# Performance work log

Hardware: AMD Instinct MI355X
Metric: run time of the kernel (lower is better)

## Reference

```python
import jax, jax.numpy as jnp
import numpy as np

N, M, E = 100000, 20000, 500000
D = 128
NNZ_E, NNZ_V = 200000, 500000


def _seg_mean(x, idx, num):
    s = jax.ops.segment_sum(x, idx, num_segments=num)
    cnt = jax.ops.segment_sum(jnp.ones((x.shape[0], 1), x.dtype), idx, num_segments=num)
    return s / jnp.maximum(cnt, 1.0)


def _spmm(row, col, val, x, num_rows):
    # COO sparse-dense matmul: out[r] = sum_nnz val * x[c]
    return jax.ops.segment_sum(val[:, None] * x[col], row, num_segments=num_rows)


def setup_inputs() -> dict:
    key = jax.random.key(0)
    ks = jax.random.split(key, 18)
    s = 0.05
    return {
        "vfeat": jax.random.normal(ks[0], (N, D), jnp.float32),
        "efeat": jax.random.normal(ks[1], (M, D), jnp.float32),
        "invDV": jax.random.uniform(ks[2], (N,), jnp.float32, 0.01, 1.0),
        "invDE": jax.random.uniform(ks[3], (M,), jnp.float32, 0.01, 1.0),
        "inc_v": jax.random.randint(ks[4], (E,), 0, N, jnp.int32),
        "inc_e": jax.random.randint(ks[5], (E,), 0, M, jnp.int32),
        "eMat_row": jax.random.randint(ks[6], (NNZ_E,), 0, M, jnp.int32),
        "eMat_col": jax.random.randint(ks[7], (NNZ_E,), 0, M, jnp.int32),
        "eMat_val": jax.random.normal(ks[8], (NNZ_E,), jnp.float32) * s,
        "vMat_row": jax.random.randint(ks[9], (NNZ_V,), 0, N, jnp.int32),
        "vMat_col": jax.random.randint(ks[10], (NNZ_V,), 0, N, jnp.int32),
        "vMat_val": jax.random.normal(ks[11], (NNZ_V,), jnp.float32) * s,
        "W_psi1": jax.random.normal(ks[12], (D, 2 * D), jnp.float32) * s,
        "b_psi1": jax.random.normal(ks[13], (D,), jnp.float32) * s,
        "W_psi2": jax.random.normal(ks[14], (D, 2 * D), jnp.float32) * s,
        "b_psi2": jax.random.normal(ks[15], (D,), jnp.float32) * s,
        "W_v": jax.random.normal(ks[16], (D, D), jnp.float32) * s,
        "W_e": jax.random.normal(ks[17], (D, D), jnp.float32) * s,
    }


def reference(vfeat, efeat, invDV, invDE, inc_v, inc_e,
              eMat_row, eMat_col, eMat_val, vMat_row, vMat_col, vMat_val,
              W_psi1, b_psi1, W_psi2, b_psi2, W_v, W_e):
    n, m = vfeat.shape[0], efeat.shape[0]
    d = vfeat.shape[1]
    # psi_1 on concat([v_src, e_dst]) per incidence. Split the concat-weight so the
    # dense GEMMs run once per node/edge instead of once per incidence (same math).
    W1v, W1e = W_psi1[:, :d], W_psi1[:, d:]
    pv1 = vfeat @ W1v.T            # [N, D]
    pe1 = efeat @ W1e.T            # [M, D]
    # psi output * src weight invDV, then mean over incident nodes per hyperedge
    psi1 = (pv1[inc_v] + pe1[inc_e] + b_psi1) * invDV[inc_v][:, None]  # [E, D]
    A = _seg_mean(psi1, inc_e, m)                                      # [M, D]
    A = _spmm(eMat_row, eMat_col, eMat_val, A, m)
    _efeat = A + efeat
    # 'con' etype: mean of incident hyperedge feats per node
    _vfeat = _seg_mean(_efeat[inc_e], inc_v, n)                        # [N, D]
    vfeat_new = jax.nn.relu(_vfeat @ W_v.T)                            # [N, D_out]
    # psi_2 on concat([v_new, e]) per incidence (no weight multiply)
    dv = vfeat_new.shape[1]
    W2v, W2e = W_psi2[:, :dv], W_psi2[:, dv:]
    psi2 = (vfeat_new @ W2v.T)[inc_v] + (efeat @ W2e.T)[inc_e] + b_psi2
    B = _seg_mean(psi2, inc_e, m)                                      # [M, D]
    _ef2 = efeat * invDE[:, None]
    _vf2 = _seg_mean(_ef2[inc_e], inc_v, n)                            # [N, D]
    _vf2 = _spmm(vMat_row, vMat_col, vMat_val, _vf2, n)
    _ef3 = _seg_mean(_vf2[inc_v], inc_e, m) + B                        # [M, D]
    efeat_new = jax.nn.relu(_ef3 @ W_e.T)
    return (vfeat_new, efeat_new)
```

## Files before the change

### kernel.cpp

```cpp
#include <hip/hip_runtime.h>

#define D 128
#define BTILE 4096

typedef __bf16 bf16;
typedef __attribute__((ext_vector_type(4))) __bf16 bf16x4;
typedef __attribute__((ext_vector_type(8))) __bf16 bf16x8;
typedef __attribute__((ext_vector_type(4))) float f32x4;
typedef __attribute__((ext_vector_type(2))) float f32x2;

__device__ __forceinline__ int pick4(int4 v, int r) {
    return r == 0 ? v.x : r == 1 ? v.y : r == 2 ? v.z : v.w;
}

#if defined(__has_builtin)
#  if __has_builtin(__builtin_amdgcn_cvt_pk_f32_fp8) && __has_builtin(__builtin_amdgcn_cvt_pk_fp8_f32)
#    define HWFP8 1
#  endif
#endif
#ifndef HWFP8
#  define HWFP8 0
#endif

__device__ __forceinline__ void dec_fp8x8(uint2 p, float* o) {
#if HWFP8
    f32x2 a = __builtin_amdgcn_cvt_pk_f32_fp8((int)p.x, false);
    f32x2 b = __builtin_amdgcn_cvt_pk_f32_fp8((int)p.x, true);
    f32x2 c = __builtin_amdgcn_cvt_pk_f32_fp8((int)p.y, false);
    f32x2 d = __builtin_amdgcn_cvt_pk_f32_fp8((int)p.y, true);
    o[0]=a.x; o[1]=a.y; o[2]=b.x; o[3]=b.y; o[4]=c.x; o[5]=c.y; o[6]=d.x; o[7]=d.y;
#else
    unsigned w0 = p.x, w1 = p.y;
#pragma unroll
    for (int k = 0; k < 8; ++k) {
        unsigned b8 = ((k < 4 ? w0 : w1) >> ((k & 3) * 8)) & 0xffu;
        unsigned bits = ((b8 & 0x80u) << 24) | ((b8 & 0x7fu) << 20);
        o[k] = __uint_as_float(bits) * 0x1p+120f;
    }
#endif
}

#if !HWFP8
__device__ __forceinline__ unsigned enc_fp8_sw(float x) {
    unsigned u = __float_as_uint(x);
    unsigned s = (u >> 24) & 0x80u;
    int e = (int)((u >> 23) & 0xffu) - 127;
    unsigned m = u & 0x7fffffu;
    if (e < -6) return s;
    unsigned mant = m >> 20;
    unsigned rest = m & 0xfffffu;
    mant += (rest > 0x80000u) || (rest == 0x80000u && (mant & 1u));
    unsigned E = (unsigned)(e + 7);
    if (mant == 8u) { mant = 0u; E += 1u; }
    if (E > 15u || (E == 15u && mant > 6u)) return s | 0x7eu;
    return s | (E << 3) | mant;
}
#endif

__device__ __forceinline__ uint2 enc_fp8x8(const float* v) {
#if HWFP8
    int lo = 0, hi = 0;
    lo = __builtin_amdgcn_cvt_pk_fp8_f32(v[0], v[1], lo, false);
    lo = __builtin_amdgcn_cvt_pk_fp8_f32(v[2], v[3], lo, true);
    hi = __builtin_amdgcn_cvt_pk_fp8_f32(v[4], v[5], hi, false);
    hi = __builtin_amdgcn_cvt_pk_fp8_f32(v[6], v[7], hi, true);
    return make_uint2((unsigned)lo, (unsigned)hi);
#else
    unsigned w0 = 0, w1 = 0;
#pragma unroll
    for (int k = 0; k < 4; ++k) w0 |= enc_fp8_sw(v[k]) << (k * 8);
#pragma unroll
    for (int k = 0; k < 4; ++k) w1 |= enc_fp8_sw(v[4 + k]) << (k * 8);
    return make_uint2(w0, w1);
#endif
}

template<int F8>
__device__ __forceinline__ void row_load(const void* src, int g, int lc, float* o) {
    if constexpr (F8) {
        uint2 p = *(const uint2*)((const unsigned char*)src + (size_t)g * D + lc * 8);
        dec_fp8x8(p, o);
    } else {
        bf16x8 p = *(const bf16x8*)((const bf16*)src + (size_t)g * D + lc * 8);
#pragma unroll
        for (int k = 0; k < 8; ++k) o[k] = (float)p[k];
    }
}

__global__ __launch_bounds__(256) void cvt_bf16(
    const float* __restrict__ in, bf16* __restrict__ out, int n4)
{
    int i = blockIdx.x * 256 + threadIdx.x;
    if (i >= n4) return;
    float4 f = ((const float4*)in)[i];
    bf16x4 v = { (bf16)f.x, (bf16)f.y, (bf16)f.z, (bf16)f.w };
    ((bf16x4*)out)[i] = v;
}

__global__ __launch_bounds__(256) void cvt_fp8(
    const float* __restrict__ in, unsigned char* __restrict__ out, int n8)
{
    int i = blockIdx.x * 256 + threadIdx.x;
    if (i >= n8) return;
    float4 f0 = *(const float4*)(in + (size_t)i * 8);
    float4 f1 = *(const float4*)(in + (size_t)i * 8 + 4);
    float v[8] = { f0.x, f0.y, f0.z, f0.w, f1.x, f1.y, f1.z, f1.w };
    *(uint2*)(out + (size_t)i * 8) = enc_fp8x8(v);
}

__global__ __launch_bounds__(256) void wfold(
    const float* __restrict__ Wv, const float* __restrict__ W1, const float* __restrict__ b1,
    const float* __restrict__ We, const float* __restrict__ W2, const float* __restrict__ b2,
    float* __restrict__ W1f, float* __restrict__ b1f,
    float* __restrict__ W2f, float* __restrict__ b2f)
{
    int gid = blockIdx.x * 256 + threadIdx.x;
    if (gid < 65536) {
        int which = gid >> 15;
        int i = (gid >> 8) & 127;
        int j = gid & 255;
        const float* A = which ? We : Wv;
        const float* B = which ? W2 : W1;
        float s = 0.0f;
        for (int k = 0; k < 128; ++k) s += A[i * 128 + k] * B[k * 256 + j];
        (which ? W2f : W1f)[i * 256 + j] = s;
    } else if (gid < 65536 + 256) {
        int t = gid - 65536, which = t >> 7, i = t & 127;
        const float* A = which ? We : Wv;
        const float* B = which ? b2 : b1;
        float s = 0.0f;
        for (int k = 0; k < 128; ++k) s += A[i * 128 + k] * B[k];
        (which ? b2f : b1f)[i] = s;
    }
}

__global__ __launch_bounds__(256) void gemm_dual(
    const bf16* __restrict__ X, const float* __restrict__ W1, const float* __restrict__ W2,
    bf16* __restrict__ o1, bf16* __restrict__ o2, int R)
{
    __shared__ __align__(16) bf16 Ws[2][D * D];
    const int t = threadIdx.x;
    for (int g = t; g < D * 16; g += 256) {
        int row = g >> 4, blk = g & 15;
        int sb = (blk ^ (row & 15)) * 8;
#pragma unroll
        for (int wsel = 0; wsel < 2; ++wsel) {
            const float* src = (wsel ? W2 : W1) + (size_t)row * D + blk * 8;
            float4 f0 = *(const float4*)(src);
            float4 f1 = *(const float4*)(src + 4);
            bf16x8 v = { (bf16)f0.x, (bf16)f0.y, (bf16)f0.z, (bf16)f0.w,
                         (bf16)f1.x, (bf16)f1.y, (bf16)f1.z, (bf16)f1.w };
            *(bf16x8*)(&Ws[wsel][row * D + sb]) = v;
        }
    }
    __syncthreads();

    const int lane = t & 63, wave = t >> 6;
    const int lrow = lane & 15, lk8 = lane >> 4;
    const int r0 = blockIdx.x * 128 + wave * 32;

    f32x4 acc[2][2][8] = {};
    for (int ks = 0; ks < 4; ++ks) {
        bf16x8 a[2];
#pragma unroll
        for (int mf = 0; mf < 2; ++mf) {
            int r = r0 + mf * 16 + lrow;
            if (r > R - 1) r = R - 1;
            a[mf] = *(const bf16x8*)(X + (size_t)r * D + ks * 32 + lk8 * 8);
        }
#pragma unroll
        for (int nf = 0; nf < 8; ++nf) {
            int row = nf * 16 + lrow;
            int blk = ks * 4 + lk8;
            int idx = row * D + (blk ^ (row & 15)) * 8;
            bf16x8 b0 = *(const bf16x8*)(&Ws[0][idx]);
            bf16x8 b1 = *(const bf16x8*)(&Ws[1][idx]);
#pragma unroll
            for (int mf = 0; mf < 2; ++mf) {
                acc[0][mf][nf] = __builtin_amdgcn_mfma_f32_16x16x32_bf16(a[mf], b0, acc[0][mf][nf], 0, 0, 0);
                acc[1][mf][nf] = __builtin_amdgcn_mfma_f32_16x16x32_bf16(a[mf], b1, acc[1][mf][nf], 0, 0, 0);
            }
        }
    }

#pragma unroll
    for (int mf = 0; mf < 2; ++mf) {
        int rbase = r0 + mf * 16 + (lane >> 4) * 4;
#pragma unroll
        for (int e = 0; e < 4; ++e) {
            int r = rbase + e;
            if (r >= R) continue;
#pragma unroll
            for (int nf = 0; nf < 8; ++nf) {
                o1[(size_t)r * D + nf * 16 + (lane & 15)] = (bf16)acc[0][mf][nf][e];
                o2[(size_t)r * D + nf * 16 + (lane & 15)] = (bf16)acc[1][mf][nf][e];
            }
        }
    }
}

__global__ __launch_bounds__(256) void gemm_psi(
    const bf16* __restrict__ X1, const bf16* __restrict__ X2,
    const float* __restrict__ rowfac, const float* __restrict__ Wf,
    const float* __restrict__ bf_, const bf16* __restrict__ addH,
    float* __restrict__ outF, bf16* __restrict__ outH, int R, int doRelu)
{
    __shared__ __align__(16) bf16 Ws[D * 256];
    const int t = threadIdx.x;
    for (int g = t; g < D * 32; g += 256) {
        int row = g >> 5, blk = g & 31;
        const float* src = Wf + (size_t)row * 256 + blk * 8;
        float4 f0 = *(const float4*)(src);
        float4 f1 = *(const float4*)(src + 4);
        bf16x8 v = { (bf16)f0.x, (bf16)f0.y, (bf16)f0.z, (bf16)f0.w,
                     (bf16)f1.x, (bf16)f1.y, (bf16)f1.z, (bf16)f1.w };
        *(bf16x8*)(&Ws[row * 256 + (blk ^ (row & 15)) * 8]) = v;
    }
    __syncthreads();

    const int lane = t & 63, wave = t >> 6;
    const int lrow = lane & 15, lk8 = lane >> 4;
    const int r0 = blockIdx.x * 128 + wave * 32;

    int rr[2]; float fac[2];
#pragma unroll
    for (int mf = 0; mf < 2; ++mf) {
        rr[mf] = min(r0 + mf * 16 + lrow, R - 1);
        fac[mf] = rowfac[rr[mf]];
    }

    f32x4 acc[2][8] = {};
    for (int ks = 0; ks < 8; ++ks) {
        bf16x8 a[2];
#pragma unroll
        for (int mf = 0; mf < 2; ++mf) {
            if (ks < 4) {
                a[mf] = *(const bf16x8*)(X1 + (size_t)rr[mf] * D + ks * 32 + lk8 * 8);
            } else {
                bf16x8 m = *(const bf16x8*)(X2 + (size_t)rr[mf] * D + (ks - 4) * 32 + lk8 * 8);
#pragma unroll
                for (int c = 0; c < 8; ++c) a[mf][c] = (bf16)((float)m[c] * fac[mf]);
            }
        }
        bf16x8 b[8];
#pragma unroll
        for (int nf = 0; nf < 8; ++nf) {
            int row = nf * 16 + lrow;
            int blk = ks * 4 + lk8;
            b[nf] = *(const bf16x8*)(&Ws[row * 256 + (blk ^ (row & 15)) * 8]);
        }
#pragma unroll
        for (int mf = 0; mf < 2; ++mf)
#pragma unroll
            for (int nf = 0; nf < 8; ++nf)
                acc[mf][nf] = __builtin_amdgcn_mfma_f32_16x16x32_bf16(a[mf], b[nf], acc[mf][nf], 0, 0, 0);
    }

#pragma unroll
    for (int mf = 0; mf < 2; ++mf) {
        int rbase = r0 + mf * 16 + (lane >> 4) * 4;
#pragma unroll
        for (int e = 0; e < 4; ++e) {
            int r = rbase + e;
            if (r >= R) continue;
            float bs = rowfac[r];
#pragma unroll
            for (int nf = 0; nf < 8; ++nf) {
                int col = nf * 16 + (lane & 15);
                float v = acc[mf][nf][e] + bs * bf_[col];
                if (addH) v += (float)addH[(size_t)r * D + col];
                if (doRelu) v = fmaxf(v, 0.0f);
                if (outF) outF[(size_t)r * D + col] = v;
                if (outH) outH[(size_t)r * D + col] = (bf16)v;
            }
        }
    }
}

__global__ __launch_bounds__(256) void coarse_hist(
    const int* __restrict__ ie, const int* __restrict__ iv,
    const int* __restrict__ er, const int* __restrict__ vr,
    int E, int nnzE, int nnzV, int4 rbb, int4 SHv, int NB, int* __restrict__ cnt_c)
{
    __shared__ int h[1024];
    const int t = threadIdx.x;
    const int TH = 2 * E + nnzE + nnzV;
    for (int i = t; i < NB; i += 256) h[i] = 0;
    __syncthreads();
    const int base = blockIdx.x * BTILE;
#pragma unroll
    for (int j = 0; j < 16; ++j) {
        int gid = base + j * 256 + t;
        if (gid >= TH) break;
        int key, r;
        if (gid < E)                 { key = ie[gid]; r = 0; }
        else if (gid < 2 * E)        { key = iv[gid - E]; r = 1; }
        else if (gid < 2 * E + nnzE) { key = er[gid - 2 * E]; r = 2; }
        else                         { key = vr[gid - 2 * E - nnzE]; r = 3; }
        atomicAdd(&h[pick4(rbb, r) + (key >> pick4(SHv, r))], 1);
    }
    __syncthreads();
    for (int i = t; i < NB; i += 256) if (h[i]) atomicAdd(&cnt_c[i], h[i]);
}

__global__ __launch_bounds__(256) void scan_small(
    const int* __restrict__ in, int n, int* __restrict__ out)
{
    __shared__ int carry, wsum[4], wpre[5];
    int t = threadIdx.x, wid = t >> 6, lane = t & 63;
    if (t == 0) carry = 0;
    __syncthreads();
    for (int base = 0; base < n; base += 256) {
        int x = (base + t < n) ? in[base + t] : 0;
        int v = x;
#pragma unroll
        for (int of = 1; of < 64; of <<= 1) {
            int u = __shfl_up(v, of, 64);
            if (lane >= of) v += u;
        }
        if (lane == 63) wsum[wid] = v;
        __syncthreads();
        if (t == 0) { int s = carry; for (int i = 0; i < 4; ++i) { wpre[i] = s; s += wsum[i]; } wpre[4] = s; }
        __syncthreads();
        if (base + t < n) out[base + t] = wpre[wid] + v - x;
        __syncthreads();
        if (t == 0) carry = wpre[4];
        __syncthreads();
    }
    if (t == 0) out[n] = carry;
}

__global__ __launch_bounds__(256) void bucket_pass(
    const int* __restrict__ ie, const int* __restrict__ iv,
    const int* __restrict__ er_r, const int* __restrict__ er_c, const float* __restrict__ er_v,
    const int* __restrict__ vr_r, const int* __restrict__ vr_c, const float* __restrict__ vr_v,
    int E, int nnzE, int nnzV,
    int4 rbb, int4 SHv, int NB,
    const int* __restrict__ coarse_off, int* __restrict__ bcur,
    int* __restrict__ bkT, float* __restrict__ wT_sh)
{
    __shared__ int h_cnt[1024];
    __shared__ int h_gb[1024];
    const int t = threadIdx.x;
    const int TH = 2 * E + nnzE + nnzV;
    const int base = blockIdx.x * BTILE;
    for (int i = t; i < NB; i += 256) h_cnt[i] = 0;
    __syncthreads();

    int pk[16], bl[16]; float wv[16];
#pragma unroll
    for (int j = 0; j < 16; ++j) {
        int gid = base + j * 256 + t;
        bl[j] = -1; wv[j] = 0.0f;
        if (gid >= TH) continue;
        int key, gs, r; float w = 0.0f;
        if (gid < E)               { key = ie[gid]; gs = iv[gid]; r = 0; }
        else if (gid < 2 * E)      { int i2 = gid - E; key = iv[i2]; gs = ie[i2]; r = 1; }
        else if (gid < 2 * E + nnzE) { int i2 = gid - 2 * E; key = er_r[i2]; gs = er_c[i2]; w = er_v[i2]; r = 2; }
        else                       { int i2 = gid - 2 * E - nnzE; key = vr_r[i2]; gs = vr_c[i2]; w = vr_v[i2]; r = 3; }
        int sh = pick4(SHv, r);
        int b = pick4(rbb, r) + (key >> sh);
        int lk = key & ((1 << sh) - 1);
        pk[j] = (lk << 17) | gs;
        int lr = atomicAdd(&h_cnt[b], 1);
        bl[j] = (b << 12) | lr;
        wv[j] = w;
    }
    __syncthreads();

    for (int b = t; b < NB; b += 256) {
        int c = h_cnt[b];
        if (c > 0) h_gb[b] = coarse_off[b] + atomicAdd(&bcur[b], c);
    }
    __syncthreads();

#pragma unroll
    for (int j = 0; j < 16; ++j) {
        if (bl[j] < 0) continue;
        int b = bl[j] >> 12, lr = bl[j] & 4095;
        int pos = h_gb[b] + lr;
        bkT[pos] = pk[j];
        if (pos >= 2 * E) wT_sh[pos] = wv[j];
    }
}

__global__ __launch_bounds__(256) void finalize_pass(
    int E, int4 rbOff, int4 rbb, int4 SHv, int4 Kkeys,
    const int* __restrict__ coarse_off, const int* __restrict__ bkT,
    const float* __restrict__ wT_sh,
    int* __restrict__ off_all, int* __restrict__ gs_all, float* __restrict__ w_sh)
{
    __shared__ int cnt_l[1024];
    __shared__ int off_l[1025];
    __shared__ int wsum[4], wpre[4];
    const int b = blockIdx.x, t = threadIdx.x;
    const int r = (b >= rbb.w) ? 3 : (b >= rbb.z) ? 2 : (b >= rbb.y) ? 1 : 0;
    const int bloc = b - pick4(rbb, r);
    const int sh = pick4(SHv, r);
    const int rb = pick4(rbOff, r);
    const int K = pick4(Kkeys, r);
    const int k0 = bloc << sh;
    const int nk = min(1 << sh, K - k0);
    const int s0 = coarse_off[b], s1 = coarse_off[b + 1];
    for (int i = t; i < nk; i += 256) cnt_l[i] = 0;
    __syncthreads();
    for (int i = s0 + t; i < s1; i += 256)
        atomicAdd(&cnt_l[bkT[i] >> 17], 1);
    __syncthreads();
    {
        const int wid = t >> 6, lane = t & 63;
        int x[4], s = 0;
#pragma unroll
        for (int j = 0; j < 4; ++j) { int i = t * 4 + j; x[j] = (i < nk) ? cnt_l[i] : 0; s += x[j]; }
        int v = s;
#pragma unroll
        for (int of = 1; of < 64; of <<= 1) {
            int u = __shfl_up(v, of, 64);
            if (lane >= of) v += u;
        }
        if (lane == 63) wsum[wid] = v;
        __syncthreads();
        if (t == 0) { int a = 0; for (int i = 0; i < 4; ++i) { wpre[i] = a; a += wsum[i]; } }
        __syncthreads();
        int pre = wpre[wid] + (v - s);
#pragma unroll
        for (int j = 0; j < 4; ++j) { int i = t * 4 + j; if (i < nk) off_l[i] = pre; pre += x[j]; }
        if (t == 0) off_l[nk] = s1 - s0;
    }
    __syncthreads();
    for (int i = t; i < nk; i += 256) off_all[rb + k0 + i] = s0 + off_l[i];
    if (t == 0 && k0 + nk == K) off_all[rb + K] = s1;
    for (int i = t; i < nk; i += 256) cnt_l[i] = 0;
    __syncthreads();
    const bool hasw = (r >= 2);
    for (int i = s0 + t; i < s1; i += 256) {
        int p = bkT[i];
        int lk = p >> 17, gs = p & 0x1FFFF;
        int lpos = off_l[lk] + atomicAdd(&cnt_l[lk], 1);
        gs_all[s0 + lpos] = gs;
        if (hasw) w_sh[s0 + lpos] = wT_sh[i];
    }
}

template<int KIND, int SRC8, int SRC28, int OUT8>
__global__ __launch_bounds__(256) void seg_gather(
    const void* __restrict__ src, const void* __restrict__ src2,
    const int* __restrict__ off, const int* __restrict__ gs_all,
    const float* __restrict__ w_sh, const float* __restrict__ gscale,
    const bf16* __restrict__ auxH,
    void* __restrict__ outH, bf16* __restrict__ outH2,
    float* __restrict__ outF, float* __restrict__ rowfac,
    float postA, float post2, float postO, int R)
{
    const int r = blockIdx.x * 16 + (threadIdx.x >> 4);
    if (r >= R) return;
    const int lc = threadIdx.x & 15;
    const int s0 = off[r], s1 = off[r + 1];
    float acc[8] = {}, acc2[8] = {};
    float sd = 0.0f;

    int s = s0;
    for (; s + 4 <= s1; s += 4) {
        int g[4]; float wv[4];
#pragma unroll
        for (int j = 0; j < 4; ++j) g[j] = gs_all[s + j];
#pragma unroll
        for (int j = 0; j < 4; ++j) {
            if (KIND == 0) wv[j] = w_sh[s + j];
            else if (KIND == 1 || KIND == 7) wv[j] = gscale[g[j]];
            else wv[j] = 1.0f;
        }
        float v0[8], v1[8], v2[8], v3[8];
        row_load<SRC8>(src, g[0], lc, v0);
        row_load<SRC8>(src, g[1], lc, v1);
        row_load<SRC8>(src, g[2], lc, v2);
        row_load<SRC8>(src, g[3], lc, v3);
        if constexpr (KIND == 7) {
            float u0[8], u1[8], u2[8], u3[8];
            row_load<SRC28>(src2, g[0], lc, u0);
            row_load<SRC28>(src2, g[1], lc, u1);
            row_load<SRC28>(src2, g[2], lc, u2);
            row_load<SRC28>(src2, g[3], lc, u3);
#pragma unroll
            for (int c = 0; c < 8; ++c) acc2[c] += u0[c] + u1[c] + u2[c] + u3[c];
            sd += wv[0] + wv[1] + wv[2] + wv[3];
        }
#pragma unroll
        for (int c = 0; c < 8; ++c)
            acc[c] += v0[c] * wv[0] + v1[c] * wv[1] + v2[c] * wv[2] + v3[c] * wv[3];
    }
    for (; s < s1; ++s) {
        int g0 = gs_all[s];
        float w = 1.0f;
        if (KIND == 0) w = w_sh[s];
        else if (KIND == 1 || KIND == 7) w = gscale[g0];
        float v0[8];
        row_load<SRC8>(src, g0, lc, v0);
#pragma unroll
        for (int c = 0; c < 8; ++c) acc[c] += v0[c] * w;
        if constexpr (KIND == 7) {
            float u0[8];
            row_load<SRC28>(src2, g0, lc, u0);
#pragma unroll
            for (int c = 0; c < 8; ++c) acc2[c] += u0[c];
            sd += w;
        }
    }

    const int cnt = s1 - s0;
    const float rs = 1.0f / (float)max(cnt, 1);

    if constexpr (KIND == 0) {
        float o[8];
#pragma unroll
        for (int c = 0; c < 8; ++c) o[c] = acc[c] * postA;
        if (auxH) {
            bf16x8 a = *(const bf16x8*)(auxH + (size_t)r * D + lc * 8);
#pragma unroll
            for (int c = 0; c < 8; ++c) o[c] += (float)a[c];
        }
        if constexpr (OUT8) {
#pragma unroll
            for (int c = 0; c < 8; ++c) o[c] *= postO;
            *(uint2*)((unsigned char*)outH + (size_t)r * D + lc * 8) = enc_fp8x8(o);
        } else {
            bf16x8 w8;
#pragma unroll
            for (int c = 0; c < 8; ++c) w8[c] = (bf16)o[c];
            *(bf16x8*)((bf16*)outH + (size_t)r * D + lc * 8) = w8;
        }
    } else if constexpr (KIND == 1 || KIND == 6) {
        float o[8];
#pragma unroll
        for (int c = 0; c < 8; ++c) o[c] = acc[c] * rs * postA;
        if constexpr (OUT8) {
#pragma unroll
            for (int c = 0; c < 8; ++c) o[c] *= postO;
            *(uint2*)((unsigned char*)outH + (size_t)r * D + lc * 8) = enc_fp8x8(o);
        } else {
            bf16x8 w8;
#pragma unroll
            for (int c = 0; c < 8; ++c) w8[c] = (bf16)o[c];
            *(bf16x8*)((bf16*)outH + (size_t)r * D + lc * 8) = w8;
        }
        if (KIND == 6 && lc == 0) rowfac[r] = (cnt > 0) ? 1.0f : 0.0f;
    } else if constexpr (KIND == 2) {
        float o[8];
#pragma unroll
        for (int c = 0; c < 8; ++c) o[c] = fmaxf(acc[c] * rs * postA, 0.0f);
        float4 o0 = { o[0], o[1], o[2], o[3] };
        float4 o1 = { o[4], o[5], o[6], o[7] };
        *(float4*)(outF + (size_t)r * D + lc * 8) = o0;
        *(float4*)(outF + (size_t)r * D + lc * 8 + 4) = o1;
        if constexpr (OUT8) {
#pragma unroll
            for (int c = 0; c < 8; ++c) o[c] *= postO;
            *(uint2*)((unsigned char*)outH + (size_t)r * D + lc * 8) = enc_fp8x8(o);
        }
    } else {
        bf16x8 w8, w2;
#pragma unroll
        for (int c = 0; c < 8; ++c) w8[c] = (bf16)(acc[c] * rs);
#pragma unroll
        for (int c = 0; c < 8; ++c) w2[c] = (bf16)(acc2[c] * rs * post2);
        *(bf16x8*)((bf16*)outH + (size_t)r * D + lc * 8) = w8;
        *(bf16x8*)(outH2 + (size_t)r * D + lc * 8) = w2;
        if (lc == 0) rowfac[r] = sd * rs;
    }
}

extern "C" void kernel_launch(void* const* d_in, const int* in_sizes, int n_in,
                              void* d_out, int out_size, void* d_ws, size_t ws_size,
                              hipStream_t stream) {
    const float* vfeat  = (const float*)d_in[0];
    const float* efeat  = (const float*)d_in[1];
    const float* invDV  = (const float*)d_in[2];
    const float* invDE  = (const float*)d_in[3];
    const int*   inc_v  = (const int*)d_in[4];
    const int*   inc_e  = (const int*)d_in[5];
    const int*   eM_row = (const int*)d_in[6];
    const int*   eM_col = (const int*)d_in[7];
    const float* eM_val = (const float*)d_in[8];
    const int*   vM_row = (const int*)d_in[9];
    const int*   vM_col = (const int*)d_in[10];
    const float* vM_val = (const float*)d_in[11];
    const float* W_psi1 = (const float*)d_in[12];
    const float* b_psi1 = (const float*)d_in[13];
    const float* W_psi2 = (const float*)d_in[14];
    const float* b_psi2 = (const float*)d_in[15];
    const float* W_v    = (const float*)d_in[16];
    const float* W_e    = (const float*)d_in[17];

    const int N = in_sizes[0] / D;
    const int M = in_sizes[1] / D;
    const int E = in_sizes[4];
    const int nnzE = in_sizes[6];
    const int nnzV = in_sizes[9];
    const int TH = 2 * E + nnzE + nnzV;

    float* out = (float*)d_out;
    float* vfeat_new = out;
    float* efeat_new = out + (size_t)N * D;

    const int T = 2 * M + 2 * N + 4;

    const float S_B = 16.0f;
    const float S_C = 64.0f;
    const float S_N = 8.0f;

    const int shE = 8, shV = 10, shEr = 9, shVr = 10;
    auto cdiv = [](int a, int b) { return (a + b - 1) / b; };
    const int nbE  = cdiv(M, 1 << shE);
    const int nbV  = cdiv(N, 1 << shV);
    const int nbEr = cdiv(M, 1 << shEr);
    const int nbVr = cdiv(N, 1 << shVr);
    const int NB = nbE + nbV + nbEr + nbVr;
    const int4 rbb   = { 0, nbE, nbE + nbV, nbE + nbV + nbEr };
    const int4 SHv   = { shE, shV, shEr, shVr };
    const int4 Kkeys = { M, N, M, N };
    const int bV  = M + 1;
    const int bEr = bV + (N + 1);
    const int bVr = bEr + (M + 1);
    const int4 rbOff = { 0, bV, bEr, bVr };

    unsigned char* nA8 = (unsigned char*)d_ws;
    unsigned char* nB8 = nA8 + (size_t)N * D;
    unsigned char* nC8 = nB8 + (size_t)N * D;
    bf16* mE  = (bf16*)(nC8 + (size_t)N * D);
    bf16* mWe = mE + (size_t)M * D;
    bf16* mV  = mWe + (size_t)M * D;
    bf16* mB  = mV + (size_t)M * D;
    bf16* mC  = mB + (size_t)M * D;
    bf16* mP  = mC + (size_t)M * D;
    bf16* mA  = mWe;
    float* W1f = (float*)(mP + (size_t)M * D);
    float* W2f = W1f + 128 * 256;
    float* b1f = W2f + 128 * 256;
    float* b2f = b1f + 128;
    float* rowfac = b2f + 128;
    int* off_all = (int*)(rowfac + M);
    int* cnt_c   = off_all + T;
    int* bcur    = cnt_c + NB;
    int* coarse_off = bcur + NB;
    int* gs_all  = coarse_off + NB + 1;
    int* bkT     = gs_all + TH;
    float* wfin  = (float*)(bkT + TH);
    float* wTst  = wfin + (nnzE + nnzV);
    float* w_sh  = wfin - (size_t)2 * E;
    float* wT_sh = wTst - (size_t)2 * E;

    int* offE  = off_all;
    int* offV  = off_all + bV;
    int* offEr = off_all + bEr;
    int* offVr = off_all + bVr;

    const dim3 TB(256);

    hipMemsetAsync(cnt_c, 0, (size_t)(2 * NB) * 4, stream);
    coarse_hist<<<cdiv(TH, BTILE), TB, 0, stream>>>(
        inc_e, inc_v, eM_row, vM_row, E, nnzE, nnzV, rbb, SHv, NB, cnt_c);
    scan_small<<<1, TB, 0, stream>>>(cnt_c, NB, coarse_off);
    bucket_pass<<<cdiv(TH, BTILE), TB, 0, stream>>>(
        inc_e, inc_v, eM_row, eM_col, eM_val, vM_row, vM_col, vM_val,
        E, nnzE, nnzV, rbb, SHv, NB, coarse_off, bcur, bkT, wT_sh);
    finalize_pass<<<NB, TB, 0, stream>>>(
        E, rbOff, rbb, SHv, Kkeys, coarse_off, bkT, wT_sh, off_all, gs_all, w_sh);

    cvt_fp8<<<cdiv(N * D / 8, 256), TB, 0, stream>>>(vfeat, nA8, N * D / 8);
    cvt_bf16<<<cdiv(M * D / 4, 256), TB, 0, stream>>>(efeat, mE, M * D / 4);
    wfold<<<257, TB, 0, stream>>>(W_v, W_psi1, b_psi1, W_e, W_psi2, b_psi2,
                                  W1f, b1f, W2f, b2f);

    gemm_dual<<<cdiv(M, 128), TB, 0, stream>>>(mE, W_e, W_v, mWe, mV, M);
    seg_gather<1, 0, 0, 1><<<cdiv(N, 16), TB, 0, stream>>>(
        mWe, nullptr, offV, gs_all, nullptr, invDE, nullptr,
        nB8, nullptr, nullptr, nullptr, 1.0f, 1.0f, S_B, N);
    seg_gather<0, 1, 0, 1><<<cdiv(N, 16), TB, 0, stream>>>(
        nB8, nullptr, offVr, gs_all, w_sh, nullptr, nullptr,
        nC8, nullptr, nullptr, nullptr, 1.0f / S_B, 1.0f, S_C, N);
    seg_gather<7, 1, 1, 0><<<cdiv(M, 16), TB, 0, stream>>>(
        nA8, nC8, offE, gs_all, nullptr, invDV, nullptr,
        mP, mC, nullptr, rowfac, 1.0f, 1.0f / S_C, 1.0f, M);
    gemm_psi<<<cdiv(M, 128), TB, 0, stream>>>(
        mP, mE, rowfac, W1f, b1f, nullptr, nullptr, mA, M, 0);
    seg_gather<0, 0, 0, 0><<<cdiv(M, 16), TB, 0, stream>>>(
        mA, nullptr, offEr, gs_all, w_sh, nullptr, mV,
        mB, nullptr, nullptr, nullptr, 1.0f, 1.0f, 1.0f, M);
    seg_gather<2, 0, 0, 1><<<cdiv(N, 16), TB, 0, stream>>>(
        mB, nullptr, offV, gs_all, nullptr, nullptr, nullptr,
        nC8, nullptr, vfeat_new, nullptr, 1.0f, 1.0f, S_N, N);
    seg_gather<6, 1, 0, 0><<<cdiv(M, 16), TB, 0, stream>>>(
        nC8, nullptr, offE, gs_all, nullptr, nullptr, nullptr,
        mP, nullptr, nullptr, rowfac, 1.0f / S_N, 1.0f, 1.0f, M);
    gemm_psi<<<cdiv(M, 128), TB, 0, stream>>>(
        mP, mE, rowfac, W2f, b2f, mC, efeat_new, nullptr, M, 1);
}
```

Before: 267.2 us.

## Store edge intermediates in scaled fp8 and interleave node fp8 buffers

The edge-side intermediates mWe and mA are now written as scaled fp8 instead of bf16. The gathers that read them decode fp8 and undo the scale. The node fp8 buffers (input features and the C/N intermediates) are interleaved into one 256-byte row, so the KIND 7 gather reads both halves from a single line per index. This halves gather traffic on the edge tensors and improves locality of the dual node gather, at the cost of more quantisation error and extra per-element fp8 encoding in the GEMM epilogues.

```diff
diff --git a/kernel.cpp b/kernel.cpp
--- a/kernel.cpp
+++ b/kernel.cpp
@@ -75,13 +75,23 @@
 #endif
 }
 
+__device__ __forceinline__ unsigned char enc_fp8_1(float x) {
+#if HWFP8
+    int v = __builtin_amdgcn_cvt_pk_fp8_f32(x, 0.0f, 0, false);
+    return (unsigned char)(v & 0xff);
+#else
+    return (unsigned char)enc_fp8_sw(x);
+#endif
+}
+
 template<int F8>
-__device__ __forceinline__ void row_load(const void* src, int g, int lc, float* o) {
+__device__ __forceinline__ void row_load(const unsigned char* src, int g, int rs, int of,
+                                         int lc, float* o) {
     if constexpr (F8) {
-        uint2 p = *(const uint2*)((const unsigned char*)src + (size_t)g * D + lc * 8);
+        uint2 p = *(const uint2*)(src + (size_t)g * rs + of + lc * 8);
         dec_fp8x8(p, o);
     } else {
-        bf16x8 p = *(const bf16x8*)((const bf16*)src + (size_t)g * D + lc * 8);
+        bf16x8 p = *(const bf16x8*)(src + (size_t)g * rs + of + lc * 16);
 #pragma unroll
         for (int k = 0; k < 8; ++k) o[k] = (float)p[k];
     }
@@ -97,15 +107,16 @@
     ((bf16x4*)out)[i] = v;
 }
 
-__global__ __launch_bounds__(256) void cvt_fp8(
-    const float* __restrict__ in, unsigned char* __restrict__ out, int n8)
+__global__ __launch_bounds__(256) void cvt_fp8s(
+    const float* __restrict__ in, unsigned char* __restrict__ out, int n8, int rs)
 {
     int i = blockIdx.x * 256 + threadIdx.x;
     if (i >= n8) return;
     float4 f0 = *(const float4*)(in + (size_t)i * 8);
     float4 f1 = *(const float4*)(in + (size_t)i * 8 + 4);
     float v[8] = { f0.x, f0.y, f0.z, f0.w, f1.x, f1.y, f1.z, f1.w };
-    *(uint2*)(out + (size_t)i * 8) = enc_fp8x8(v);
+    int row = i >> 4, lane = i & 15;
+    *(uint2*)(out + (size_t)row * rs + lane * 8) = enc_fp8x8(v);
 }
 
 __global__ __launch_bounds__(256) void wfold(
@@ -136,7 +147,7 @@
 
 __global__ __launch_bounds__(256) void gemm_dual(
     const bf16* __restrict__ X, const float* __restrict__ W1, const float* __restrict__ W2,
-    bf16* __restrict__ o1, bf16* __restrict__ o2, int R)
+    unsigned char* __restrict__ o1, float s1, bf16* __restrict__ o2, int R)
 {
     __shared__ __align__(16) bf16 Ws[2][D * D];
     const int t = threadIdx.x;
@@ -192,8 +203,9 @@
             if (r >= R) continue;
 #pragma unroll
             for (int nf = 0; nf < 8; ++nf) {
-                o1[(size_t)r * D + nf * 16 + (lane & 15)] = (bf16)acc[0][mf][nf][e];
-                o2[(size_t)r * D + nf * 16 + (lane & 15)] = (bf16)acc[1][mf][nf][e];
+                int col = nf * 16 + (lane & 15);
+                o1[(size_t)r * D + col] = enc_fp8_1(acc[0][mf][nf][e] * s1);
+                o2[(size_t)r * D + col] = (bf16)acc[1][mf][nf][e];
             }
         }
     }
@@ -203,7 +215,8 @@
     const bf16* __restrict__ X1, const bf16* __restrict__ X2,
     const float* __restrict__ rowfac, const float* __restrict__ Wf,
     const float* __restrict__ bf_, const bf16* __restrict__ addH,
-    float* __restrict__ outF, bf16* __restrict__ outH, int R, int doRelu)
+    float* __restrict__ outF, unsigned char* __restrict__ out8, float s8,
+    int R, int doRelu)
 {
     __shared__ __align__(16) bf16 Ws[D * 256];
     const int t = threadIdx.x;
@@ -271,7 +284,7 @@
                 if (addH) v += (float)addH[(size_t)r * D + col];
                 if (doRelu) v = fmaxf(v, 0.0f);
                 if (outF) outF[(size_t)r * D + col] = v;
-                if (outH) outH[(size_t)r * D + col] = (bf16)v;
+                if (out8) out8[(size_t)r * D + col] = enc_fp8_1(v * s8);
             }
         }
     }
@@ -444,11 +457,13 @@
 
 template<int KIND, int SRC8, int SRC28, int OUT8>
 __global__ __launch_bounds__(256) void seg_gather(
-    const void* __restrict__ src, const void* __restrict__ src2,
+    const unsigned char* __restrict__ src, int rsS, int ofS,
+    const unsigned char* __restrict__ src2, int rsS2, int ofS2,
     const int* __restrict__ off, const int* __restrict__ gs_all,
     const float* __restrict__ w_sh, const float* __restrict__ gscale,
     const bf16* __restrict__ auxH,
-    void* __restrict__ outH, bf16* __restrict__ outH2,
+    unsigned char* __restrict__ outH, int rsO, int ofO,
+    bf16* __restrict__ outH2,
     float* __restrict__ outF, float* __restrict__ rowfac,
     float postA, float post2, float postO, int R)
 {
@@ -471,16 +486,16 @@
             else wv[j] = 1.0f;
         }
         float v0[8], v1[8], v2[8], v3[8];
-        row_load<SRC8>(src, g[0], lc, v0);
-        row_load<SRC8>(src, g[1], lc, v1);
-        row_load<SRC8>(src, g[2], lc, v2);
-        row_load<SRC8>(src, g[3], lc, v3);
+        row_load<SRC8>(src, g[0], rsS, ofS, lc, v0);
+        row_load<SRC8>(src, g[1], rsS, ofS, lc, v1);
+        row_load<SRC8>(src, g[2], rsS, ofS, lc, v2);
+        row_load<SRC8>(src, g[3], rsS, ofS, lc, v3);
         if constexpr (KIND == 7) {
             float u0[8], u1[8], u2[8], u3[8];
-            row_load<SRC28>(src2, g[0], lc, u0);
-            row_load<SRC28>(src2, g[1], lc, u1);
-            row_load<SRC28>(src2, g[2], lc, u2);
-            row_load<SRC28>(src2, g[3], lc, u3);
+            row_load<SRC28>(src2, g[0], rsS2, ofS2, lc, u0);
+            row_load<SRC28>(src2, g[1], rsS2, ofS2, lc, u1);
+            row_load<SRC28>(src2, g[2], rsS2, ofS2, lc, u2);
+            row_load<SRC28>(src2, g[3], rsS2, ofS2, lc, u3);
 #pragma unroll
             for (int c = 0; c < 8; ++c) acc2[c] += u0[c] + u1[c] + u2[c] + u3[c];
             sd += wv[0] + wv[1] + wv[2] + wv[3];
@@ -495,12 +510,12 @@
         if (KIND == 0) w = w_sh[s];
         else if (KIND == 1 || KIND == 7) w = gscale[g0];
         float v0[8];
-        row_load<SRC8>(src, g0, lc, v0);
+        row_load<SRC8>(src, g0, rsS, ofS, lc, v0);
 #pragma unroll
         for (int c = 0; c < 8; ++c) acc[c] += v0[c] * w;
         if constexpr (KIND == 7) {
             float u0[8];
-            row_load<SRC28>(src2, g0, lc, u0);
+            row_load<SRC28>(src2, g0, rsS2, ofS2, lc, u0);
 #pragma unroll
             for (int c = 0; c < 8; ++c) acc2[c] += u0[c];
             sd += w;
@@ -522,12 +537,12 @@
         if constexpr (OUT8) {
 #pragma unroll
             for (int c = 0; c < 8; ++c) o[c] *= postO;
-            *(uint2*)((unsigned char*)outH + (size_t)r * D + lc * 8) = enc_fp8x8(o);
+            *(uint2*)(outH + (size_t)r * rsO + ofO + lc * 8) = enc_fp8x8(o);
         } else {
             bf16x8 w8;
 #pragma unroll
             for (int c = 0; c < 8; ++c) w8[c] = (bf16)o[c];
-            *(bf16x8*)((bf16*)outH + (size_t)r * D + lc * 8) = w8;
+            *(bf16x8*)(outH + (size_t)r * 256 + lc * 16) = w8;
         }
     } else if constexpr (KIND == 1 || KIND == 6) {
         float o[8];
@@ -536,12 +551,12 @@
         if constexpr (OUT8) {
 #pragma unroll
             for (int c = 0; c < 8; ++c) o[c] *= postO;
-            *(uint2*)((unsigned char*)outH + (size_t)r * D + lc * 8) = enc_fp8x8(o);
+            *(uint2*)(outH + (size_t)r * rsO + ofO + lc * 8) = enc_fp8x8(o);
         } else {
             bf16x8 w8;
 #pragma unroll
             for (int c = 0; c < 8; ++c) w8[c] = (bf16)o[c];
-            *(bf16x8*)((bf16*)outH + (size_t)r * D + lc * 8) = w8;
+            *(bf16x8*)(outH + (size_t)r * 256 + lc * 16) = w8;
         }
         if (KIND == 6 && lc == 0) rowfac[r] = (cnt > 0) ? 1.0f : 0.0f;
     } else if constexpr (KIND == 2) {
@@ -555,7 +570,7 @@
         if constexpr (OUT8) {
 #pragma unroll
             for (int c = 0; c < 8; ++c) o[c] *= postO;
-            *(uint2*)((unsigned char*)outH + (size_t)r * D + lc * 8) = enc_fp8x8(o);
+            *(uint2*)(outH + (size_t)r * rsO + ofO + lc * 8) = enc_fp8x8(o);
         }
     } else {
         bf16x8 w8, w2;
@@ -563,7 +578,7 @@
         for (int c = 0; c < 8; ++c) w8[c] = (bf16)(acc[c] * rs);
 #pragma unroll
         for (int c = 0; c < 8; ++c) w2[c] = (bf16)(acc2[c] * rs * post2);
-        *(bf16x8*)((bf16*)outH + (size_t)r * D + lc * 8) = w8;
+        *(bf16x8*)(outH + (size_t)r * 256 + lc * 16) = w8;
         *(bf16x8*)(outH2 + (size_t)r * D + lc * 8) = w2;
         if (lc == 0) rowfac[r] = sd * rs;
     }
@@ -607,6 +622,8 @@
     const float S_B = 16.0f;
     const float S_C = 64.0f;
     const float S_N = 8.0f;
+    const float S_W = 8.0f;
+    const float S_A = 16.0f;
 
     const int shE = 8, shV = 10, shEr = 9, shVr = 10;
     auto cdiv = [](int a, int b) { return (a + b - 1) / b; };
@@ -623,16 +640,15 @@
     const int bVr = bEr + (M + 1);
     const int4 rbOff = { 0, bV, bEr, bVr };
 
-    unsigned char* nA8 = (unsigned char*)d_ws;
-    unsigned char* nB8 = nA8 + (size_t)N * D;
-    unsigned char* nC8 = nB8 + (size_t)N * D;
-    bf16* mE  = (bf16*)(nC8 + (size_t)N * D);
-    bf16* mWe = mE + (size_t)M * D;
-    bf16* mV  = mWe + (size_t)M * D;
+    unsigned char* nP8 = (unsigned char*)d_ws;
+    unsigned char* nB8 = nP8 + (size_t)N * 256;
+    bf16* mE  = (bf16*)(nB8 + (size_t)N * 128);
+    unsigned char* mWe8 = (unsigned char*)(mE + (size_t)M * D);
+    bf16* mV  = (bf16*)(mWe8 + (size_t)M * 128);
     bf16* mB  = mV + (size_t)M * D;
     bf16* mC  = mB + (size_t)M * D;
     bf16* mP  = mC + (size_t)M * D;
-    bf16* mA  = mWe;
+    unsigned char* mA8 = mWe8;
     float* W1f = (float*)(mP + (size_t)M * D);
     float* W2f = W1f + 128 * 256;
     float* b1f = W2f + 128 * 256;
@@ -666,32 +682,32 @@
     finalize_pass<<<NB, TB, 0, stream>>>(
         E, rbOff, rbb, SHv, Kkeys, coarse_off, bkT, wT_sh, off_all, gs_all, w_sh);
 
-    cvt_fp8<<<cdiv(N * D / 8, 256), TB, 0, stream>>>(vfeat, nA8, N * D / 8);
+    cvt_fp8s<<<cdiv(N * D / 8, 256), TB, 0, stream>>>(vfeat, nP8, N * D / 8, 256);
     cvt_bf16<<<cdiv(M * D / 4, 256), TB, 0, stream>>>(efeat, mE, M * D / 4);
     wfold<<<257, TB, 0, stream>>>(W_v, W_psi1, b_psi1, W_e, W_psi2, b_psi2,
                                   W1f, b1f, W2f, b2f);
 
-    gemm_dual<<<cdiv(M, 128), TB, 0, stream>>>(mE, W_e, W_v, mWe, mV, M);
-    seg_gather<1, 0, 0, 1><<<cdiv(N, 16), TB, 0, stream>>>(
-        mWe, nullptr, offV, gs_all, nullptr, invDE, nullptr,
-        nB8, nullptr, nullptr, nullptr, 1.0f, 1.0f, S_B, N);
+    gemm_dual<<<cdiv(M, 128), TB, 0, stream>>>(mE, W_e, W_v, mWe8, S_W, mV, M);
+    seg_gather<1, 1, 0, 1><<<cdiv(N, 16), TB, 0, stream>>>(
+        mWe8, 128, 0, nullptr, 0, 0, offV, gs_all, nullptr, invDE, nullptr,
+        nB8, 128, 0, nullptr, nullptr, nullptr, 1.0f / S_W, 1.0f, S_B, N);
     seg_gather<0, 1, 0, 1><<<cdiv(N, 16), TB, 0, stream>>>(
-        nB8, nullptr, offVr, gs_all, w_sh, nullptr, nullptr,
-        nC8, nullptr, nullptr, nullptr, 1.0f / S_B, 1.0f, S_C, N);
+        nB8, 128, 0, nullptr, 0, 0, offVr, gs_all, w_sh, nullptr, nullptr,
+        nP8, 256, 128, nullptr, nullptr, nullptr, 1.0f / S_B, 1.0f, S_C, N);
     seg_gather<7, 1, 1, 0><<<cdiv(M, 16), TB, 0, stream>>>(
-        nA8, nC8, offE, gs_all, nullptr, invDV, nullptr,
-        mP, mC, nullptr, rowfac, 1.0f, 1.0f / S_C, 1.0f, M);
+        nP8, 256, 0, nP8, 256, 128, offE, gs_all, nullptr, invDV, nullptr,
+        (unsigned char*)mP, 256, 0, mC, nullptr, rowfac, 1.0f, 1.0f / S_C, 1.0f, M);
     gemm_psi<<<cdiv(M, 128), TB, 0, stream>>>(
-        mP, mE, rowfac, W1f, b1f, nullptr, nullptr, mA, M, 0);
-    seg_gather<0, 0, 0, 0><<<cdiv(M, 16), TB, 0, stream>>>(
-        mA, nullptr, offEr, gs_all, w_sh, nullptr, mV,
-        mB, nullptr, nullptr, nullptr, 1.0f, 1.0f, 1.0f, M);
+        mP, mE, rowfac, W1f, b1f, nullptr, nullptr, mA8, S_A, M, 0);
+    seg_gather<0, 1, 0, 0><<<cdiv(M, 16), TB, 0, stream>>>(
+        mA8, 128, 0, nullptr, 0, 0, offEr, gs_all, w_sh, nullptr, mV,
+        (unsigned char*)mB, 256, 0, nullptr, nullptr, nullptr, 1.0f / S_A, 1.0f, 1.0f, M);
     seg_gather<2, 0, 0, 1><<<cdiv(N, 16), TB, 0, stream>>>(
-        mB, nullptr, offV, gs_all, nullptr, nullptr, nullptr,
-        nC8, nullptr, vfeat_new, nullptr, 1.0f, 1.0f, S_N, N);
+        (unsigned char*)mB, 256, 0, nullptr, 0, 0, offV, gs_all, nullptr, nullptr, nullptr,
+        nP8, 256, 128, nullptr, vfeat_new, nullptr, 1.0f, 1.0f, S_N, N);
     seg_gather<6, 1, 0, 0><<<cdiv(M, 16), TB, 0, stream>>>(
-        nC8, nullptr, offE, gs_all, nullptr, nullptr, nullptr,
-        mP, nullptr, nullptr, rowfac, 1.0f / S_N, 1.0f, 1.0f, M);
+        nP8, 256, 128, nullptr, 0, 0, offE, gs_all, nullptr, nullptr, nullptr,
+        (unsigned char*)mP, 256, 0, nullptr, nullptr, rowfac, 1.0f / S_N, 1.0f, 1.0f, M);
     gemm_psi<<<cdiv(M, 128), TB, 0, stream>>>(
-        mP, mE, rowfac, W2f, b2f, mC, efeat_new, nullptr, M, 1);
-}
+        mP, mE, rowfac, W2f, b2f, mC, efeat_new, nullptr, 1.0f, M, 1);
+}
```

Result: no change. 263.9 us (-1.3%).
